# Performance work log

Hardware: AMD Instinct MI355X
Metric: run time of the kernel (lower is better)

## Reference

```python
import jax, jax.numpy as jnp
import numpy as np

N_TOKENS = 2097152
N_FEATURES = 64
N_MODELS = 64
N_LAYERS = 4


def setup_inputs() -> dict:
    key = jax.random.key(0)
    k1, k2, k3 = jax.random.split(key, 3)
    x = jax.random.normal(k1, (N_TOKENS, N_FEATURES), dtype=jnp.float32)
    # Packed per-model Linear params, torch convention: weight [out, in]
    scale = 1.0 / np.sqrt(N_FEATURES)
    W = jax.random.normal(k2, (N_MODELS, N_LAYERS, N_FEATURES, N_FEATURES), dtype=jnp.float32) * scale
    b = jax.random.normal(k3, (N_MODELS, N_LAYERS, N_FEATURES), dtype=jnp.float32) * scale
    return {"x": x, "W": W, "b": b}


def reference(x, W, b):
    # x: [N, d]; rows are partitioned into N_MODELS equal contiguous slices.
    # W: [M, L, d_out, d_in], b: [M, L, d_out]
    n, d = x.shape
    xg = x.reshape(N_MODELS, n // N_MODELS, d)  # [M, n_per, d]
    for l in range(N_LAYERS):
        # torch Linear: y = x @ W.T + b, per model (grouped GEMM)
        xg = jnp.einsum('mnd,mfd->mnf', xg, W[:, l]) + b[:, l][:, None, :]
        xg = jax.nn.relu(xg)
    return xg.reshape(n, d)
```

## Files before the change

### kernel.cpp

```cpp
#include <hip/hip_runtime.h>


typedef __attribute__((ext_vector_type(8))) _Float16 f16x8;
typedef __attribute__((ext_vector_type(2))) __fp16 fp16x2;
typedef __attribute__((ext_vector_type(4))) float f32x4;

#define MODELS 64
#define LAYERS 4
#define DIM 64
#define TOKS_PER_MODEL 32768
#define BLOCKS_PER_MODEL 16
#define WAVES_PER_BLOCK 4
#define TOK_PER_WAVE (TOKS_PER_MODEL / (BLOCKS_PER_MODEL * WAVES_PER_BLOCK))
#define TILE_TOKS 32
#define TILES_PER_WAVE (TOK_PER_WAVE / TILE_TOKS)

#define WF_BYTES (LAYERS * 4 * 2 * 64 * 16)
#define BIAS_OFF WF_BYTES
#define LDS_BYTES (WF_BYTES + LAYERS * DIM * 4)

union H8 { f16x8 v; fp16x2 h2[4]; };

#define LOAD4(D0, D1, D2, D3, P)                                   \
    {                                                              \
        D0 = *(const f32x4*)((P) + 0);                             \
        D1 = *(const f32x4*)((P) + 16);                            \
        D2 = *(const f32x4*)((P) + 32);                            \
        D3 = *(const f32x4*)((P) + 48);                            \
    }

#define CVT_Z(Z0, Z1, X0, X1, X2, X3)                              \
    {                                                              \
        H8 z0u_, z1u_;                                             \
        z0u_.h2[0] = __builtin_amdgcn_cvt_pkrtz(X0[0], X0[1]);     \
        z0u_.h2[1] = __builtin_amdgcn_cvt_pkrtz(X0[2], X0[3]);     \
        z0u_.h2[2] = __builtin_amdgcn_cvt_pkrtz(X1[0], X1[1]);     \
        z0u_.h2[3] = __builtin_amdgcn_cvt_pkrtz(X1[2], X1[3]);     \
        z1u_.h2[0] = __builtin_amdgcn_cvt_pkrtz(X2[0], X2[1]);     \
        z1u_.h2[1] = __builtin_amdgcn_cvt_pkrtz(X2[2], X2[3]);     \
        z1u_.h2[2] = __builtin_amdgcn_cvt_pkrtz(X3[0], X3[1]);     \
        z1u_.h2[3] = __builtin_amdgcn_cvt_pkrtz(X3[2], X3[3]);     \
        Z0 = z0u_.v; Z1 = z1u_.v;                                  \
    }

#define REPACK(Z0, Z1, ACC)                                                  \
    {                                                                        \
        H8 n0_, n1_;                                                         \
        _Pragma("unroll")                                                    \
        for (int t_ = 0; t_ < 2; ++t_) {                                     \
            n0_.h2[t_ * 2 + 0] = __builtin_amdgcn_cvt_pkrtz(                 \
                fmaxf(ACC[t_][0], 0.0f), fmaxf(ACC[t_][1], 0.0f));           \
            n0_.h2[t_ * 2 + 1] = __builtin_amdgcn_cvt_pkrtz(                 \
                fmaxf(ACC[t_][2], 0.0f), fmaxf(ACC[t_][3], 0.0f));           \
            n1_.h2[t_ * 2 + 0] = __builtin_amdgcn_cvt_pkrtz(                 \
                fmaxf(ACC[2 + t_][0], 0.0f), fmaxf(ACC[2 + t_][1], 0.0f));   \
            n1_.h2[t_ * 2 + 1] = __builtin_amdgcn_cvt_pkrtz(                 \
                fmaxf(ACC[2 + t_][2], 0.0f), fmaxf(ACC[2 + t_][3], 0.0f));   \
        }                                                                    \
        Z0 = n0_.v; Z1 = n1_.v;                                              \
    }

__global__ __launch_bounds__(256, 2) void mlp4_fused(
    const float* __restrict__ x, const float* __restrict__ W,
    const float* __restrict__ b, float* __restrict__ out) {

    __shared__ __align__(16) unsigned char smem[LDS_BYTES];

    const int lane = threadIdx.x & 63;
    const int wave = threadIdx.x >> 6;
    const int c = lane & 15;
    const int g = lane >> 4;

    const int m   = blockIdx.x / BLOCKS_PER_MODEL;
    const int blk = blockIdx.x % BLOCKS_PER_MODEL;
    const size_t tok0 = (size_t)m * TOKS_PER_MODEL
                      + (size_t)(blk * WAVES_PER_BLOCK + wave) * TOK_PER_WAVE;

    {
        const int l = wave;
        const float* Wl = W + ((size_t)m * LAYERS + l) * DIM * DIM;
        #pragma unroll
        for (int t = 0; t < 4; ++t) {
            const float* row = Wl + (size_t)(t * 16 + c) * DIM + 4 * g;
            f32x4 c0 = *(const f32x4*)(row + 0);
            f32x4 c1 = *(const f32x4*)(row + 16);
            f32x4 c2 = *(const f32x4*)(row + 32);
            f32x4 c3 = *(const f32x4*)(row + 48);
            H8 a0, a1;
            #pragma unroll
            for (int e = 0; e < 4; ++e) {
                a0.v[e]     = (_Float16)c0[e];
                a0.v[4 + e] = (_Float16)c1[e];
                a1.v[e]     = (_Float16)c2[e];
                a1.v[4 + e] = (_Float16)c3[e];
            }
            *(f16x8*)(smem + ((size_t)((l * 4 + t) * 2 + 0) * 1024) + lane * 16) = a0.v;
            *(f16x8*)(smem + ((size_t)((l * 4 + t) * 2 + 1) * 1024) + lane * 16) = a1.v;
        }
        if (lane < 16) {
            const float* bl = b + ((size_t)m * LAYERS + l) * DIM + lane * 4;
            *(f32x4*)(smem + BIAS_OFF + l * 256 + lane * 16) = *(const f32x4*)bl;
        }
    }
    __syncthreads();

    const float* xp = x   + tok0 * DIM + (size_t)(c * DIM + 4 * g);
    float*       op = out + tok0 * DIM + (size_t)(c * DIM + 4 * g);

    f32x4 XA0, XA1, XA2, XA3, XB0, XB1, XB2, XB3;
    LOAD4(XA0, XA1, XA2, XA3, xp + 0 * (16 * DIM));
    LOAD4(XB0, XB1, XB2, XB3, xp + 1 * (16 * DIM));

    #pragma unroll 1
    for (int tile = 0; tile < TILES_PER_WAVE; ++tile) {
        f16x8 zA0, zA1, zB0, zB1;
        CVT_Z(zA0, zA1, XA0, XA1, XA2, XA3);
        CVT_Z(zB0, zB1, XB0, XB1, XB2, XB3);

        const int nxt = (tile + 1) & (TILES_PER_WAVE - 1);
        const float* nx = xp + (size_t)nxt * (TILE_TOKS * DIM);
        LOAD4(XA0, XA1, XA2, XA3, nx + 0 * (16 * DIM));
        LOAD4(XB0, XB1, XB2, XB3, nx + 1 * (16 * DIM));

        f32x4 accA[4], accB[4];
        #pragma unroll
        for (int l = 0; l < LAYERS; ++l) {
            #pragma unroll
            for (int t = 0; t < 4; ++t) {
                f32x4 bv = *(const f32x4*)(smem + BIAS_OFF + l * 256 + t * 64 + g * 16);
                accA[t] = bv;
                accB[t] = bv;
            }
            #pragma unroll
            for (int t = 0; t < 4; ++t) {
                f16x8 w0 = *(const f16x8*)(smem + ((size_t)((l * 4 + t) * 2 + 0) * 1024) + lane * 16);
                accA[t] = __builtin_amdgcn_mfma_f32_16x16x32_f16(w0, zA0, accA[t], 0, 0, 0);
                accB[t] = __builtin_amdgcn_mfma_f32_16x16x32_f16(w0, zB0, accB[t], 0, 0, 0);
            }
            #pragma unroll
            for (int t = 0; t < 4; ++t) {
                f16x8 w1 = *(const f16x8*)(smem + ((size_t)((l * 4 + t) * 2 + 1) * 1024) + lane * 16);
                accA[t] = __builtin_amdgcn_mfma_f32_16x16x32_f16(w1, zA1, accA[t], 0, 0, 0);
                accB[t] = __builtin_amdgcn_mfma_f32_16x16x32_f16(w1, zB1, accB[t], 0, 0, 0);
            }
            if (l < LAYERS - 1) {
                REPACK(zA0, zA1, accA);
                REPACK(zB0, zB1, accB);
            }
        }

        float* oA = op + (size_t)tile * (TILE_TOKS * DIM);
        float* oB = oA + 16 * DIM;
        #pragma unroll
        for (int t = 0; t < 4; ++t) {
            f32x4 rA, rB;
            #pragma unroll
            for (int r = 0; r < 4; ++r) {
                rA[r] = fmaxf(accA[t][r], 0.0f);
                rB[r] = fmaxf(accB[t][r], 0.0f);
            }
            *(f32x4*)(oA + t * 16) = rA;
            *(f32x4*)(oB + t * 16) = rB;
        }
    }
}

extern "C" void kernel_launch(void* const* d_in, const int* in_sizes, int n_in,
                              void* d_out, int out_size, void* d_ws, size_t ws_size,
                              hipStream_t stream) {
    (void)in_sizes; (void)n_in; (void)out_size; (void)d_ws; (void)ws_size;
    const float* x = (const float*)d_in[0];
    const float* W = (const float*)d_in[1];
    const float* b = (const float*)d_in[2];
    float* out = (float*)d_out;
    mlp4_fused<<<dim3(MODELS * BLOCKS_PER_MODEL), dim3(256), 0, stream>>>(x, W, b, out);
}
```

Baseline: 241.3 us.

## Use 512-thread blocks and interleave token tiles across waves

Blocks grow to 8 waves, and each model is covered by half as many blocks. Each wave now handles a strided set of 32-token tiles spaced by the total wave count, instead of one contiguous chunk, so concurrently running waves touch adjacent memory. Weight staging is split so each pair of waves loads one layer. The aim is better DRAM locality and coalescing across waves and less per-block weight-staging overhead, at the cost of larger blocks that may limit occupancy.

```diff
diff --git a/kernel.cpp b/kernel.cpp
--- a/kernel.cpp
+++ b/kernel.cpp
@@ -9,11 +9,13 @@
 #define LAYERS 4
 #define DIM 64
 #define TOKS_PER_MODEL 32768
-#define BLOCKS_PER_MODEL 16
-#define WAVES_PER_BLOCK 4
-#define TOK_PER_WAVE (TOKS_PER_MODEL / (BLOCKS_PER_MODEL * WAVES_PER_BLOCK))
+#define THREADS 512
+#define WAVES_PER_BLOCK 8
+#define BLOCKS_PER_MODEL 8
+#define WAVES_PER_MODEL (BLOCKS_PER_MODEL * WAVES_PER_BLOCK)
 #define TILE_TOKS 32
-#define TILES_PER_WAVE (TOK_PER_WAVE / TILE_TOKS)
+#define STEPS (TOKS_PER_MODEL / (WAVES_PER_MODEL * TILE_TOKS))
+#define STEP_FLOATS ((size_t)WAVES_PER_MODEL * TILE_TOKS * DIM)
 
 #define WF_BYTES (LAYERS * 4 * 2 * 64 * 16)
 #define BIAS_OFF WF_BYTES
@@ -60,7 +62,7 @@
         Z0 = n0_.v; Z1 = n1_.v;                                              \
     }
 
-__global__ __launch_bounds__(256, 2) void mlp4_fused(
+__global__ __launch_bounds__(THREADS, 2) void mlp4_fused(
     const float* __restrict__ x, const float* __restrict__ W,
     const float* __restrict__ b, float* __restrict__ out) {
 
@@ -73,14 +75,15 @@
 
     const int m   = blockIdx.x / BLOCKS_PER_MODEL;
     const int blk = blockIdx.x % BLOCKS_PER_MODEL;
-    const size_t tok0 = (size_t)m * TOKS_PER_MODEL
-                      + (size_t)(blk * WAVES_PER_BLOCK + wave) * TOK_PER_WAVE;
+    const int q   = blk * WAVES_PER_BLOCK + wave;
 
     {
-        const int l = wave;
+        const int l = wave >> 1;
+        const int tbase = (wave & 1) * 2;
         const float* Wl = W + ((size_t)m * LAYERS + l) * DIM * DIM;
         #pragma unroll
-        for (int t = 0; t < 4; ++t) {
+        for (int ti = 0; ti < 2; ++ti) {
+            const int t = tbase + ti;
             const float* row = Wl + (size_t)(t * 16 + c) * DIM + 4 * g;
             f32x4 c0 = *(const f32x4*)(row + 0);
             f32x4 c1 = *(const f32x4*)(row + 16);
@@ -97,28 +100,30 @@
             *(f16x8*)(smem + ((size_t)((l * 4 + t) * 2 + 0) * 1024) + lane * 16) = a0.v;
             *(f16x8*)(smem + ((size_t)((l * 4 + t) * 2 + 1) * 1024) + lane * 16) = a1.v;
         }
-        if (lane < 16) {
+        if ((wave & 1) == 0 && lane < 16) {
             const float* bl = b + ((size_t)m * LAYERS + l) * DIM + lane * 4;
             *(f32x4*)(smem + BIAS_OFF + l * 256 + lane * 16) = *(const f32x4*)bl;
         }
     }
     __syncthreads();
 
-    const float* xp = x   + tok0 * DIM + (size_t)(c * DIM + 4 * g);
-    float*       op = out + tok0 * DIM + (size_t)(c * DIM + 4 * g);
+    const float* xp = x   + ((size_t)m * TOKS_PER_MODEL + (size_t)q * TILE_TOKS) * DIM
+                          + (size_t)(c * DIM + 4 * g);
+    float*       op = out + ((size_t)m * TOKS_PER_MODEL + (size_t)q * TILE_TOKS) * DIM
+                          + (size_t)(c * DIM + 4 * g);
 
     f32x4 XA0, XA1, XA2, XA3, XB0, XB1, XB2, XB3;
     LOAD4(XA0, XA1, XA2, XA3, xp + 0 * (16 * DIM));
     LOAD4(XB0, XB1, XB2, XB3, xp + 1 * (16 * DIM));
 
     #pragma unroll 1
-    for (int tile = 0; tile < TILES_PER_WAVE; ++tile) {
+    for (int s = 0; s < STEPS; ++s) {
         f16x8 zA0, zA1, zB0, zB1;
         CVT_Z(zA0, zA1, XA0, XA1, XA2, XA3);
         CVT_Z(zB0, zB1, XB0, XB1, XB2, XB3);
 
-        const int nxt = (tile + 1) & (TILES_PER_WAVE - 1);
-        const float* nx = xp + (size_t)nxt * (TILE_TOKS * DIM);
+        const int nxt = (s + 1) & (STEPS - 1);
+        const float* nx = xp + (size_t)nxt * STEP_FLOATS;
         LOAD4(XA0, XA1, XA2, XA3, nx + 0 * (16 * DIM));
         LOAD4(XB0, XB1, XB2, XB3, nx + 1 * (16 * DIM));
 
@@ -149,7 +154,7 @@
             }
         }
 
-        float* oA = op + (size_t)tile * (TILE_TOKS * DIM);
+        float* oA = op + (size_t)s * STEP_FLOATS;
         float* oB = oA + 16 * DIM;
         #pragma unroll
         for (int t = 0; t < 4; ++t) {
@@ -173,5 +178,5 @@
     const float* W = (const float*)d_in[1];
     const float* b = (const float*)d_in[2];
     float* out = (float*)d_out;
-    mlp4_fused<<<dim3(MODELS * BLOCKS_PER_MODEL), dim3(256), 0, stream>>>(x, W, b, out);
+    mlp4_fused<<<dim3(MODELS * BLOCKS_PER_MODEL), dim3(THREADS), 0, stream>>>(x, W, b, out);
 }
```

After: 241.3 us. No clear change (+0.0%).
